# Optimization experiments

Measured on AMD Instinct MI355X. Metric: run time of the kernel, lower is better.

Reference implementation:

```python
import jax, jax.numpy as jnp
import numpy as np

N = 50000
E = 800000
F_IN, H1, H2, C = 512, 256, 32, 16


def _glorot(key, shape):
    lim = float(np.sqrt(6.0 / (shape[0] + shape[1])))
    return jax.random.uniform(key, shape, jnp.float32, -lim, lim)


def setup_inputs() -> dict:
    key = jax.random.key(0)
    ks = jax.random.split(key, 8)
    x = jax.random.normal(ks[0], (N, F_IN), jnp.float32)
    edge_index = jax.random.randint(ks[1], (2, E), 0, N, jnp.int64)
    return {
        "x": x,
        "edge_index": edge_index,
        "W1": _glorot(ks[2], (F_IN, H1)), "b1": jnp.zeros((H1,), jnp.float32),
        "W2": _glorot(ks[3], (H1, H2)), "b2": jnp.zeros((H2,), jnp.float32),
        "W3": _glorot(ks[4], (H2, C)), "b3": jnp.zeros((C,), jnp.float32),
    }


def _gcn_norm(edge_index, n_nodes):
    # Add self-loops, compute symmetric normalization deg^-1/2[src]*deg^-1/2[dst]
    loop = jnp.arange(n_nodes, dtype=edge_index.dtype)
    src = jnp.concatenate([edge_index[0], loop])
    dst = jnp.concatenate([edge_index[1], loop])
    ones = jnp.ones(src.shape[0], jnp.float32)
    deg = jax.ops.segment_sum(ones, dst, num_segments=n_nodes)
    dinv = jnp.where(deg > 0, jax.lax.rsqrt(deg), 0.0)
    norm = dinv[src] * dinv[dst]  # [E+N]
    return src, dst, norm


def _gcn_conv(x, W, b, src, dst, norm, n_nodes):
    h = x @ W  # transform first (reduces scatter width)
    msg = h[src] * norm[:, None]  # gather + scale, [E+N, out]
    out = jax.ops.segment_sum(msg, dst, num_segments=n_nodes)
    return out + b


def reference(x, edge_index, W1, b1, W2, b2, W3, b3):
    n_nodes = x.shape[0]
    src, dst, norm = _gcn_norm(edge_index, n_nodes)
    h = _gcn_conv(x, W1, b1, src, dst, norm, n_nodes)
    h = jax.nn.relu(h)  # dropout is identity in eval mode
    h = _gcn_conv(h, W2, b2, src, dst, norm, n_nodes)
    h = jax.nn.relu(h)
    h = _gcn_conv(h, W3, b3, src, dst, norm, n_nodes)
    return h
```

## Files before the change

### kernel.cpp

```cpp
#include <hip/hip_runtime.h>

constexpr int N   = 50000;
constexpr int E   = 800000;
constexpr int FIN = 512;
constexpr int H1v = 256;
constexpr int H2v = 32;
constexpr int Cv  = 16;

constexpr int NBLK = (N + 1023) / 1024;

typedef __attribute__((ext_vector_type(8))) short short8;
typedef __attribute__((ext_vector_type(4))) float f32x4;
typedef __attribute__((ext_vector_type(4))) unsigned short us4;
typedef __attribute__((ext_vector_type(8))) unsigned short us8;
typedef __attribute__((ext_vector_type(4))) unsigned int uint4v;

__device__ inline unsigned short f2bf(float f) {
    unsigned u = __float_as_uint(f);
    return (unsigned short)((u + 0x7FFFu + ((u >> 16) & 1u)) >> 16);
}
__device__ inline float bf2f(unsigned short b) { return __uint_as_float(((unsigned)b) << 16); }


__global__ __launch_bounds__(256) void k_init(const float* __restrict__ W,
                                              unsigned short* __restrict__ Wf,
                                              int* __restrict__ cnt) {
    const int b = blockIdx.x;
    if (b < 64) {
        int t = b * 256 + threadIdx.x;
        int l = t & 63, nt = (t >> 6) & 15, kt = t >> 10;
        int n = nt * 16 + (l & 15);
        int kb = kt * 32 + (l >> 4) * 8;
        short8 h8, l8;
#pragma unroll
        for (int j = 0; j < 8; ++j) {
            float w = W[(size_t)(kb + j) * H1v + n];
            unsigned short h = f2bf(w);
            h8[j] = (short)h;
            l8[j] = (short)f2bf(w - bf2f(h));
        }
        size_t base = ((size_t)(kt * 16 + nt) * 2) * 512 + (size_t)l * 8;
        *(short8*)(Wf + base) = h8;
        *(short8*)(Wf + base + 512) = l8;
    } else {
        int i = (b - 64) * 256 + threadIdx.x;
        if (i <= N) cnt[i] = 0;
    }
}


__global__ __launch_bounds__(256) void k_hist(const int* __restrict__ dst,
                                              int* __restrict__ cnt) {
    int e = blockIdx.x * 256 + threadIdx.x;
    if (e < E) atomicAdd(&cnt[dst[e]], 1);
}

__global__ __launch_bounds__(256) void k_scan_part(const int* __restrict__ cnt,
                                                   int* __restrict__ bsum) {
    __shared__ int red[256];
    const int t = threadIdx.x;
    const int base = blockIdx.x * 1024 + t * 4;
    int s = 0;
#pragma unroll
    for (int i = 0; i < 4; ++i) {
        int idx = base + i;
        if (idx < N) s += cnt[idx];
    }
    red[t] = s;
    __syncthreads();
    for (int off = 128; off > 0; off >>= 1) {
        if (t < off) red[t] += red[t + off];
        __syncthreads();
    }
    if (t == 0) bsum[blockIdx.x] = red[0];
}

__global__ __launch_bounds__(256) void k_scan_final(const int* __restrict__ cnt,
                                                    const int* __restrict__ bsum,
                                                    int* __restrict__ row_ptr,
                                                    int* __restrict__ cursor,
                                                    float* __restrict__ dinv) {
    __shared__ int sums[256];
    __shared__ int s_bofs, s_tot;
    const int t = threadIdx.x;

    if (t < 64) {
        int v = (t < NBLK) ? bsum[t] : 0;
        int pre = (t < (int)blockIdx.x) ? v : 0;
#pragma unroll
        for (int off = 32; off > 0; off >>= 1) {
            pre += __shfl_down(pre, off, 64);
            v   += __shfl_down(v, off, 64);
        }
        if (t == 0) { s_bofs = pre; s_tot = v; }
    }

    const int base = blockIdx.x * 1024 + t * 4;
    int v[4];
    int local = 0;
#pragma unroll
    for (int i = 0; i < 4; ++i) {
        int idx = base + i;
        v[i] = (idx < N) ? cnt[idx] : 0;
        local += v[i];
    }
    sums[t] = local;
    __syncthreads();
    for (int off = 1; off < 256; off <<= 1) {
        int u = (t >= off) ? sums[t - off] : 0;
        __syncthreads();
        sums[t] += u;
        __syncthreads();
    }
    int run = s_bofs + sums[t] - local;
#pragma unroll
    for (int i = 0; i < 4; ++i) {
        int idx = base + i;
        if (idx < N) {
            row_ptr[idx] = run;
            cursor[idx] = run;
            dinv[idx] = rsqrtf(1.0f + (float)v[i]);
        }
        run += v[i];
    }
    if (blockIdx.x == NBLK - 1 && t == 0) row_ptr[N] = s_tot;
}

__global__ __launch_bounds__(256) void k_permute(const int* __restrict__ src,
                                                 const int* __restrict__ dst,
                                                 int* __restrict__ cursor,
                                                 int* __restrict__ srcs) {
    int e = blockIdx.x * 256 + threadIdx.x;
    if (e < E) {
        int pos = atomicAdd(&cursor[dst[e]], 1);
        srcs[pos] = src[e];
    }
}


__device__ inline void split_pair(float x0, float x1, unsigned& hp, unsigned& lp) {
    unsigned u0 = __float_as_uint(x0), u1 = __float_as_uint(x1);
    unsigned h0 = u0 & 0xffff0000u, h1 = u1 & 0xffff0000u;
    float l0 = x0 - __uint_as_float(h0);
    float l1 = x1 - __uint_as_float(h1);
    hp = __builtin_amdgcn_perm(u1, u0, 0x07060302u);
    lp = __builtin_amdgcn_perm(__float_as_uint(l1), __float_as_uint(l0), 0x07060302u);
}

__device__ inline void split_frag(const float4& a, const float4& b, short8& hi, short8& lo) {
    unsigned h0, h1, h2, h3, l0, l1, l2, l3;
    split_pair(a.x, a.y, h0, l0);
    split_pair(a.z, a.w, h1, l1);
    split_pair(b.x, b.y, h2, l2);
    split_pair(b.z, b.w, h3, l3);
    uint4v h, l;
    h[0] = h0; h[1] = h1; h[2] = h2; h[3] = h3;
    l[0] = l0; l[1] = l1; l[2] = l2; l[3] = l3;
    hi = __builtin_bit_cast(short8, h);
    lo = __builtin_bit_cast(short8, l);
}

__device__ inline void stage_x_tile(const float* __restrict__ X, int brow, int k0,
                                    float* lds, int tid) {
    const int wbase = tid & ~63;
#pragma unroll
    for (int c = 0; c < 4; ++c) {
        int q = c * 256 + tid;
        int row = q >> 4;
        int gc = ((q & 15) ^ (row & 15)) << 2;
        int r = brow + row;
        const float* src = X + (size_t)(r < N ? r : 0) * FIN + k0 + gc;
        float* dst = lds + (size_t)(c * 256 + wbase) * 4;
        __builtin_amdgcn_global_load_lds((const __attribute__((address_space(1))) void*)src,
                                         (__attribute__((address_space(3))) void*)dst,
                                         16, 0, 0);
    }
}

__global__ __launch_bounds__(256, 4) void k_gemm1_mfma(const float* __restrict__ X,
                                                       const unsigned short* __restrict__ Wf,
                                                       const float* __restrict__ dinv,
                                                       unsigned short* __restrict__ Hout) {
    __shared__ float As[2][4096];
    const int tid = threadIdx.x;
    const int w = tid >> 6, l = tid & 63;
    const int wr = w >> 1, wc = w & 1;
    const int brow = blockIdx.x * 64;
    const int row0 = brow + wr * 32;
    const int wrow = wr * 32;
    const int colb = blockIdx.y;
    const int lm = l & 15;
    const int lk2 = (l >> 4) * 2;

    const unsigned short* bp0 = Wf + (size_t)(colb * 8 + wc * 4) * 1024 + (size_t)l * 8;

    f32x4 acc[2][4];
#pragma unroll
    for (int i = 0; i < 2; ++i)
#pragma unroll
        for (int j = 0; j < 4; ++j) acc[i][j] = (f32x4)0.f;

    stage_x_tile(X, brow, 0, As[0], tid);

    for (int kt = 0; kt < 8; ++kt) {
        const int cur = kt & 1;
        __syncthreads();

        const unsigned short* bpA = bp0 + (size_t)(2 * kt) * 16384;
        short8 B0h[4], B0l[4];
#pragma unroll
        for (int j = 0; j < 4; ++j) {
            B0h[j] = *(const short8*)(bpA + j * 1024);
            B0l[j] = *(const short8*)(bpA + j * 1024 + 512);
        }

        if (kt < 7) stage_x_tile(X, brow, (kt + 1) * 64, As[cur ^ 1], tid);

        const float* Ab = As[cur];

        short8 Ah[2], Al[2];
#pragma unroll
        for (int i = 0; i < 2; ++i) {
            int row = wrow + i * 16 + lm;
            const float* rbp = Ab + row * 64;
            int p = row & 15;
            float4 a0 = *(const float4*)(rbp + ((lk2 ^ p) << 2));
            float4 a1 = *(const float4*)(rbp + (((lk2 + 1) ^ p) << 2));
            split_frag(a0, a1, Ah[i], Al[i]);
        }

        const unsigned short* bpB = bpA + 16384;
        short8 B1h[4], B1l[4];
#pragma unroll
        for (int j = 0; j < 4; ++j) {
            B1h[j] = *(const short8*)(bpB + j * 1024);
            B1l[j] = *(const short8*)(bpB + j * 1024 + 512);
        }

#pragma unroll
        for (int i = 0; i < 2; ++i)
#pragma unroll
            for (int j = 0; j < 4; ++j) {
                acc[i][j] = __builtin_amdgcn_mfma_f32_16x16x32_bf16(Ah[i], B0h[j], acc[i][j], 0, 0, 0);
                acc[i][j] = __builtin_amdgcn_mfma_f32_16x16x32_bf16(Ah[i], B0l[j], acc[i][j], 0, 0, 0);
                acc[i][j] = __builtin_amdgcn_mfma_f32_16x16x32_bf16(Al[i], B0h[j], acc[i][j], 0, 0, 0);
            }

#pragma unroll
        for (int i = 0; i < 2; ++i) {
            int row = wrow + i * 16 + lm;
            const float* rbp = Ab + row * 64;
            int p = row & 15;
            int g0 = lk2 + 8;
            float4 a0 = *(const float4*)(rbp + ((g0 ^ p) << 2));
            float4 a1 = *(const float4*)(rbp + (((g0 + 1) ^ p) << 2));
            split_frag(a0, a1, Ah[i], Al[i]);
        }

#pragma unroll
        for (int i = 0; i < 2; ++i)
#pragma unroll
            for (int j = 0; j < 4; ++j) {
                acc[i][j] = __builtin_amdgcn_mfma_f32_16x16x32_bf16(Ah[i], B1h[j], acc[i][j], 0, 0, 0);
                acc[i][j] = __builtin_amdgcn_mfma_f32_16x16x32_bf16(Ah[i], B1l[j], acc[i][j], 0, 0, 0);
                acc[i][j] = __builtin_amdgcn_mfma_f32_16x16x32_bf16(Al[i], B1h[j], acc[i][j], 0, 0, 0);
            }
    }

    const int col0 = colb * 128 + wc * 64;
#pragma unroll
    for (int i = 0; i < 2; ++i) {
        int rbase = row0 + i * 16 + (l >> 4) * 4;
        float dv[4];
        bool okr[4];
#pragma unroll
        for (int r = 0; r < 4; ++r) {
            int rr = rbase + r;
            okr[r] = rr < N;
            dv[r] = okr[r] ? dinv[rr] : 0.f;
        }
#pragma unroll
        for (int j = 0; j < 4; ++j) {
            int col = col0 + j * 16 + lm;
#pragma unroll
            for (int r = 0; r < 4; ++r)
                if (okr[r]) Hout[(size_t)(rbase + r) * H1v + col] = f2bf(acc[i][j][r] * dv[r]);
        }
    }
}


__global__ __launch_bounds__(256) void k_gemm2(const float* __restrict__ A,
                                               const float* __restrict__ W,
                                               const float* __restrict__ dinv,
                                               unsigned short* __restrict__ Hout) {
    __shared__ float Ws[H1v * H2v];
    const int tid = threadIdx.x;
#pragma unroll
    for (int i = 0; i < 8; ++i) {
        int off = tid * 4 + i * 1024;
        *(float4*)(&Ws[off]) = *(const float4*)(W + off);
    }
    __syncthreads();

    const int row = blockIdx.x * 8 + (tid >> 5);
    const int col = tid & 31;
    if (row >= N) return;
    const float* arow = A + (size_t)row * H1v;
    float sum = 0.f;
#pragma unroll 4
    for (int k = 0; k < H1v; k += 4) {
        float4 a4 = *(const float4*)(arow + k);
        sum = fmaf(a4.x, Ws[(k + 0) * H2v + col], sum);
        sum = fmaf(a4.y, Ws[(k + 1) * H2v + col], sum);
        sum = fmaf(a4.z, Ws[(k + 2) * H2v + col], sum);
        sum = fmaf(a4.w, Ws[(k + 3) * H2v + col], sum);
    }
    Hout[(size_t)row * H2v + col] = f2bf(sum * dinv[row]);
}


__global__ __launch_bounds__(256) void k_agg_d256(const unsigned short* __restrict__ h,
                                                  const int* __restrict__ rp,
                                                  const int* __restrict__ srcs,
                                                  const float* __restrict__ dinv,
                                                  const float* __restrict__ bias,
                                                  float* __restrict__ out) {
    const int half = threadIdx.x >> 5;
    const int lane = threadIdx.x & 31;
    const int d = blockIdx.x * 8 + half;
    if (d >= N) return;
    const int beg = rp[d], end = rp[d + 1];
    const int fo = lane * 8;
    const unsigned short* hb = h + fo;
    us8 sv = *(const us8*)(hb + (size_t)d * H1v);
    float a[8];
#pragma unroll
    for (int q = 0; q < 8; ++q) a[q] = bf2f(sv[q]);
    int j = beg;
    for (; j + 3 < end; j += 4) {
        int s0 = srcs[j], s1 = srcs[j + 1], s2 = srcs[j + 2], s3 = srcs[j + 3];
        us8 v0 = *(const us8*)(hb + (size_t)s0 * H1v);
        us8 v1 = *(const us8*)(hb + (size_t)s1 * H1v);
        us8 v2 = *(const us8*)(hb + (size_t)s2 * H1v);
        us8 v3 = *(const us8*)(hb + (size_t)s3 * H1v);
#pragma unroll
        for (int q = 0; q < 8; ++q)
            a[q] += bf2f(v0[q]) + bf2f(v1[q]) + bf2f(v2[q]) + bf2f(v3[q]);
    }
    for (; j < end; ++j) {
        us8 v = *(const us8*)(hb + (size_t)srcs[j] * H1v);
#pragma unroll
        for (int q = 0; q < 8; ++q) a[q] += bf2f(v[q]);
    }
    const float di = dinv[d];
    const float4 b0 = *(const float4*)(bias + fo);
    const float4 b1 = *(const float4*)(bias + fo + 4);
    float4 o0, o1;
    o0.x = fmaxf(fmaf(di, a[0], b0.x), 0.f);
    o0.y = fmaxf(fmaf(di, a[1], b0.y), 0.f);
    o0.z = fmaxf(fmaf(di, a[2], b0.z), 0.f);
    o0.w = fmaxf(fmaf(di, a[3], b0.w), 0.f);
    o1.x = fmaxf(fmaf(di, a[4], b1.x), 0.f);
    o1.y = fmaxf(fmaf(di, a[5], b1.y), 0.f);
    o1.z = fmaxf(fmaf(di, a[6], b1.z), 0.f);
    o1.w = fmaxf(fmaf(di, a[7], b1.w), 0.f);
    *(float4*)(out + (size_t)d * H1v + fo) = o0;
    *(float4*)(out + (size_t)d * H1v + fo + 4) = o1;
}


__global__ __launch_bounds__(256) void k_agg32_gemm3(const unsigned short* __restrict__ h2,
                                                     const int* __restrict__ rp,
                                                     const int* __restrict__ srcs,
                                                     const float* __restrict__ dinv,
                                                     const float* __restrict__ b2,
                                                     const float* __restrict__ W3,
                                                     unsigned short* __restrict__ h3) {
    __shared__ float als[16][33];
    __shared__ float W3s[H2v * Cv];
    const int t = threadIdx.x;
    *(float2*)(&W3s[t * 2]) = *(const float2*)(W3 + t * 2);

    const int sub = t >> 4, fg = t & 15;
    const int d = blockIdx.x * 16 + sub;
    const int beg = rp[d], end = rp[d + 1];
    const unsigned short* h2b = h2 + fg * 2;
    unsigned sv = *(const unsigned*)(h2b + (size_t)d * H2v);
    float a0 = __uint_as_float(sv << 16);
    float a1 = __uint_as_float(sv & 0xffff0000u);
    int j = beg;
    for (; j + 3 < end; j += 4) {
        unsigned v0 = *(const unsigned*)(h2b + (size_t)srcs[j] * H2v);
        unsigned v1 = *(const unsigned*)(h2b + (size_t)srcs[j + 1] * H2v);
        unsigned v2 = *(const unsigned*)(h2b + (size_t)srcs[j + 2] * H2v);
        unsigned v3 = *(const unsigned*)(h2b + (size_t)srcs[j + 3] * H2v);
        a0 += __uint_as_float(v0 << 16) + __uint_as_float(v1 << 16)
            + __uint_as_float(v2 << 16) + __uint_as_float(v3 << 16);
        a1 += __uint_as_float(v0 & 0xffff0000u) + __uint_as_float(v1 & 0xffff0000u)
            + __uint_as_float(v2 & 0xffff0000u) + __uint_as_float(v3 & 0xffff0000u);
    }
    for (; j < end; ++j) {
        unsigned v = *(const unsigned*)(h2b + (size_t)srcs[j] * H2v);
        a0 += __uint_as_float(v << 16);
        a1 += __uint_as_float(v & 0xffff0000u);
    }
    const float di = dinv[d];
    als[sub][fg * 2]     = fmaxf(fmaf(di, a0, b2[fg * 2]), 0.f);
    als[sub][fg * 2 + 1] = fmaxf(fmaf(di, a1, b2[fg * 2 + 1]), 0.f);
    __syncthreads();

    const int row = t >> 4, col = t & 15;
    float sum = 0.f;
#pragma unroll
    for (int k = 0; k < H2v; ++k) sum = fmaf(als[row][k], W3s[k * Cv + col], sum);
    const int gr = blockIdx.x * 16 + row;
    h3[(size_t)gr * Cv + col] = f2bf(sum * dinv[gr]);
}


__global__ __launch_bounds__(256) void k_agg16(const unsigned short* __restrict__ h,
                                               const int* __restrict__ rp,
                                               const int* __restrict__ srcs,
                                               const float* __restrict__ dinv,
                                               const float* __restrict__ bias,
                                               float* __restrict__ out) {
    const int sub = threadIdx.x >> 3;
    const int fg = threadIdx.x & 7;
    const int d = blockIdx.x * 32 + sub;
    if (d >= N) return;
    const int beg = rp[d], end = rp[d + 1];
    const unsigned short* hb = h + fg * 2;
    unsigned sv = *(const unsigned*)(hb + (size_t)d * Cv);
    float a0 = __uint_as_float(sv << 16);
    float a1 = __uint_as_float(sv & 0xffff0000u);
    int j = beg;
    for (; j + 3 < end; j += 4) {
        unsigned v0 = *(const unsigned*)(hb + (size_t)srcs[j] * Cv);
        unsigned v1 = *(const unsigned*)(hb + (size_t)srcs[j + 1] * Cv);
        unsigned v2 = *(const unsigned*)(hb + (size_t)srcs[j + 2] * Cv);
        unsigned v3 = *(const unsigned*)(hb + (size_t)srcs[j + 3] * Cv);
        a0 += __uint_as_float(v0 << 16) + __uint_as_float(v1 << 16)
            + __uint_as_float(v2 << 16) + __uint_as_float(v3 << 16);
        a1 += __uint_as_float(v0 & 0xffff0000u) + __uint_as_float(v1 & 0xffff0000u)
            + __uint_as_float(v2 & 0xffff0000u) + __uint_as_float(v3 & 0xffff0000u);
    }
    for (; j < end; ++j) {
        unsigned v = *(const unsigned*)(hb + (size_t)srcs[j] * Cv);
        a0 += __uint_as_float(v << 16);
        a1 += __uint_as_float(v & 0xffff0000u);
    }
    const float di = dinv[d];
    float2 o;
    o.x = fmaf(di, a0, bias[fg * 2]);
    o.y = fmaf(di, a1, bias[fg * 2 + 1]);
    *(float2*)(out + (size_t)d * Cv + fg * 2) = o;
}


extern "C" void kernel_launch(void* const* d_in, const int* in_sizes, int n_in,
                              void* d_out, int out_size, void* d_ws, size_t ws_size,
                              hipStream_t stream) {
    const float* x  = (const float*)d_in[0];
    const int*   ei = (const int*)d_in[1];
    const float* W1 = (const float*)d_in[2];
    const float* b1 = (const float*)d_in[3];
    const float* W2 = (const float*)d_in[4];
    const float* b2 = (const float*)d_in[5];
    const float* W3 = (const float*)d_in[6];
    const float* b3 = (const float*)d_in[7];
    const int* src = ei;
    const int* dst = ei + E;
    float* out = (float*)d_out;

    char* ws = (char*)d_ws;
    float* dinv   = (float*)ws;
    int*   cnt    = (int*)(ws + 0x40000);
    int*   rp     = cnt;
    int*   cursor = (int*)(ws + 0x80000);
    int*   bsum   = (int*)(ws + 0xB2000);
    int*   srcs   = (int*)(ws + 0xC0000);
    unsigned short* wsplit = (unsigned short*)(ws + (size_t)4 * 1024 * 1024);
    char* p = ws + (size_t)5 * 1024 * 1024;
    unsigned short* h1 = (unsigned short*)p; p += (size_t)N * H1v * sizeof(unsigned short);
    float*          a1 = (float*)p;          p += (size_t)N * H1v * sizeof(float);
    unsigned short* h2 = (unsigned short*)p; p += (size_t)N * H2v * sizeof(unsigned short);
    unsigned short* h3 = (unsigned short*)p;

    k_init<<<64 + (N + 256) / 256, 256, 0, stream>>>(W1, wsplit, cnt);
    k_hist<<<(E + 255) / 256, 256, 0, stream>>>(dst, cnt);
    k_scan_part<<<NBLK, 256, 0, stream>>>(cnt, bsum);
    k_scan_final<<<NBLK, 256, 0, stream>>>(cnt, bsum, rp, cursor, dinv);
    k_permute<<<(E + 255) / 256, 256, 0, stream>>>(src, dst, cursor, srcs);

    dim3 g1((N + 63) / 64, 2);
    k_gemm1_mfma<<<g1, 256, 0, stream>>>(x, wsplit, dinv, h1);
    k_agg_d256<<<(N + 7) / 8, 256, 0, stream>>>(h1, rp, srcs, dinv, b1, a1);

    k_gemm2<<<N / 8, 256, 0, stream>>>(a1, W2, dinv, h2);

    k_agg32_gemm3<<<N / 16, 256, 0, stream>>>(h2, rp, srcs, dinv, b2, W3, h3);

    k_agg16<<<(N + 31) / 32, 256, 0, stream>>>(h3, rp, srcs, dinv, b3, out);
}
```

Measured before the change: 425.9 us.

## Split gemm1 into chunked launches, register-block gemm2 rows, widen agg unroll

GEMM1 now runs as four launches of 196x2 blocks, each covering a slice of 12544 rows (4*12544 = 50176, so the tail is covered), which changes scheduling and wave quantization. GEMM2 gives each thread four rows, so every LDS weight read is reused across four accumulators and the grid shrinks fourfold. The 256-wide aggregation gathers eight neighbours per iteration instead of four, putting more loads in flight, at the cost of more registers. The extra launches add some launch overhead.

```diff
diff --git a/kernel.cpp b/kernel.cpp
--- a/kernel.cpp
+++ b/kernel.cpp
@@ -180,12 +180,13 @@
 __global__ __launch_bounds__(256, 4) void k_gemm1_mfma(const float* __restrict__ X,
                                                        const unsigned short* __restrict__ Wf,
                                                        const float* __restrict__ dinv,
-                                                       unsigned short* __restrict__ Hout) {
+                                                       unsigned short* __restrict__ Hout,
+                                                       int browBase) {
     __shared__ float As[2][4096];
     const int tid = threadIdx.x;
     const int w = tid >> 6, l = tid & 63;
     const int wr = w >> 1, wc = w & 1;
-    const int brow = blockIdx.x * 64;
+    const int brow = browBase + blockIdx.x * 64;
     const int row0 = brow + wr * 32;
     const int wrow = wr * 32;
     const int colb = blockIdx.y;
@@ -303,20 +304,37 @@
     }
     __syncthreads();
 
-    const int row = blockIdx.x * 8 + (tid >> 5);
+    const int r0 = blockIdx.x * 32 + (tid >> 5);
     const int col = tid & 31;
-    if (row >= N) return;
-    const float* arow = A + (size_t)row * H1v;
-    float sum = 0.f;
-#pragma unroll 4
+    const float* arow = A + (size_t)r0 * H1v;
+    bool ok[4];
+    float sum[4];
+#pragma unroll
+    for (int i = 0; i < 4; ++i) { ok[i] = (r0 + 8 * i) < N; sum[i] = 0.f; }
+#pragma unroll 2
     for (int k = 0; k < H1v; k += 4) {
-        float4 a4 = *(const float4*)(arow + k);
-        sum = fmaf(a4.x, Ws[(k + 0) * H2v + col], sum);
-        sum = fmaf(a4.y, Ws[(k + 1) * H2v + col], sum);
-        sum = fmaf(a4.z, Ws[(k + 2) * H2v + col], sum);
-        sum = fmaf(a4.w, Ws[(k + 3) * H2v + col], sum);
-    }
-    Hout[(size_t)row * H2v + col] = f2bf(sum * dinv[row]);
+        float4 a4[4];
+#pragma unroll
+        for (int i = 0; i < 4; ++i)
+            a4[i] = ok[i] ? *(const float4*)(arow + (size_t)(8 * i) * H1v + k)
+                          : make_float4(0.f, 0.f, 0.f, 0.f);
+        float w0 = Ws[(k + 0) * H2v + col];
+        float w1 = Ws[(k + 1) * H2v + col];
+        float w2 = Ws[(k + 2) * H2v + col];
+        float w3 = Ws[(k + 3) * H2v + col];
+#pragma unroll
+        for (int i = 0; i < 4; ++i) {
+            sum[i] = fmaf(a4[i].x, w0, sum[i]);
+            sum[i] = fmaf(a4[i].y, w1, sum[i]);
+            sum[i] = fmaf(a4[i].z, w2, sum[i]);
+            sum[i] = fmaf(a4[i].w, w3, sum[i]);
+        }
+    }
+#pragma unroll
+    for (int i = 0; i < 4; ++i) {
+        int r = r0 + 8 * i;
+        if (ok[i]) Hout[(size_t)r * H2v + col] = f2bf(sum[i] * dinv[r]);
+    }
 }
 
 
@@ -338,12 +356,25 @@
 #pragma unroll
     for (int q = 0; q < 8; ++q) a[q] = bf2f(sv[q]);
     int j = beg;
+    for (; j + 7 < end; j += 8) {
+        us8 v0 = *(const us8*)(hb + (size_t)srcs[j] * H1v);
+        us8 v1 = *(const us8*)(hb + (size_t)srcs[j + 1] * H1v);
+        us8 v2 = *(const us8*)(hb + (size_t)srcs[j + 2] * H1v);
+        us8 v3 = *(const us8*)(hb + (size_t)srcs[j + 3] * H1v);
+        us8 v4 = *(const us8*)(hb + (size_t)srcs[j + 4] * H1v);
+        us8 v5 = *(const us8*)(hb + (size_t)srcs[j + 5] * H1v);
+        us8 v6 = *(const us8*)(hb + (size_t)srcs[j + 6] * H1v);
+        us8 v7 = *(const us8*)(hb + (size_t)srcs[j + 7] * H1v);
+#pragma unroll
+        for (int q = 0; q < 8; ++q)
+            a[q] += ((bf2f(v0[q]) + bf2f(v1[q])) + (bf2f(v2[q]) + bf2f(v3[q])))
+                  + ((bf2f(v4[q]) + bf2f(v5[q])) + (bf2f(v6[q]) + bf2f(v7[q])));
+    }
     for (; j + 3 < end; j += 4) {
-        int s0 = srcs[j], s1 = srcs[j + 1], s2 = srcs[j + 2], s3 = srcs[j + 3];
-        us8 v0 = *(const us8*)(hb + (size_t)s0 * H1v);
-        us8 v1 = *(const us8*)(hb + (size_t)s1 * H1v);
-        us8 v2 = *(const us8*)(hb + (size_t)s2 * H1v);
-        us8 v3 = *(const us8*)(hb + (size_t)s3 * H1v);
+        us8 v0 = *(const us8*)(hb + (size_t)srcs[j] * H1v);
+        us8 v1 = *(const us8*)(hb + (size_t)srcs[j + 1] * H1v);
+        us8 v2 = *(const us8*)(hb + (size_t)srcs[j + 2] * H1v);
+        us8 v3 = *(const us8*)(hb + (size_t)srcs[j + 3] * H1v);
 #pragma unroll
         for (int q = 0; q < 8; ++q)
             a[q] += bf2f(v0[q]) + bf2f(v1[q]) + bf2f(v2[q]) + bf2f(v3[q]);
@@ -493,11 +524,12 @@
     k_scan_final<<<NBLK, 256, 0, stream>>>(cnt, bsum, rp, cursor, dinv);
     k_permute<<<(E + 255) / 256, 256, 0, stream>>>(src, dst, cursor, srcs);
 
-    dim3 g1((N + 63) / 64, 2);
-    k_gemm1_mfma<<<g1, 256, 0, stream>>>(x, wsplit, dinv, h1);
+    dim3 g1(196, 2);
+    for (int c = 0; c < 4; ++c)
+        k_gemm1_mfma<<<g1, 256, 0, stream>>>(x, wsplit, dinv, h1, c * 12544);
     k_agg_d256<<<(N + 7) / 8, 256, 0, stream>>>(h1, rp, srcs, dinv, b1, a1);
 
-    k_gemm2<<<N / 8, 256, 0, stream>>>(a1, W2, dinv, h2);
+    k_gemm2<<<(N + 31) / 32, 256, 0, stream>>>(a1, W2, dinv, h2);
 
     k_agg32_gemm3<<<N / 16, 256, 0, stream>>>(h2, rp, srcs, dinv, b2, W3, h3);
 
```

Result: slower. 509.2 us (+19.6%).
